# Kernel optimization log

Measured on AMD Instinct MI355X. Metric: run time of the kernel, lower is better.

Reference implementation:

```python
import jax, jax.numpy as jnp
import numpy as np

N_NODES = 100000
N_EDGES = 3200000


def _spmm(edge_row, edge_col, edge_val, h):
    # out[i] = sum_{e: row[e]==i} val[e] * h[col[e]]
    msgs = edge_val[:, None] * h[edge_col]  # [E, F]
    return jax.ops.segment_sum(msgs, edge_row, num_segments=N_NODES)


def _gc_layer(x, W, b, edge_row, edge_col, edge_val):
    # GraphConvolution: support = x @ W; out = spmm(adj, support) + b
    support = x @ W
    return _spmm(edge_row, edge_col, edge_val, support) + b


def setup_inputs() -> dict:
    key = jax.random.key(0)
    ks = jax.random.split(key, 8)
    F_IN, HID, C = 512, 256, 40
    x = jax.random.normal(ks[0], (N_NODES, F_IN), dtype=jnp.float32)
    W1 = jax.random.normal(ks[1], (F_IN, HID), dtype=jnp.float32) * (1.0 / np.sqrt(F_IN))
    b1 = jnp.zeros((HID,), dtype=jnp.float32)
    W2 = jax.random.normal(ks[2], (HID, C), dtype=jnp.float32) * (1.0 / np.sqrt(HID))
    b2 = jnp.zeros((C,), dtype=jnp.float32)
    edge_row = jax.random.randint(ks[3], (N_EDGES,), 0, N_NODES, dtype=jnp.int32)
    edge_col = jax.random.randint(ks[4], (N_EDGES,), 0, N_NODES, dtype=jnp.int32)
    edge_val = jax.random.uniform(ks[5], (N_EDGES,), dtype=jnp.float32) * 0.05
    return {"x": x, "W1": W1, "b1": b1, "W2": W2, "b2": b2,
            "edge_row": edge_row, "edge_col": edge_col, "edge_val": edge_val}


def reference(x, W1, b1, W2, b2, edge_row, edge_col, edge_val):
    h = jax.nn.relu(_gc_layer(x, W1, b1, edge_row, edge_col, edge_val))
    # dropout: inference mode (training=False) -> identity
    logits = _gc_layer(h, W2, b2, edge_row, edge_col, edge_val)
    return (jax.nn.log_softmax(logits, axis=1), jax.nn.softmax(logits, axis=1))
```

## Files before the change

### kernel.cpp

```cpp
#include <hip/hip_runtime.h>
#include <hip/hip_bf16.h>

#define N_NODES 100000
#define N_EDGES 3200000
#define F_IN    512
#define HID     256
#define C_OUT   40

#define RPB     512
#define BSHIFT  9
#define NBUCK   196
#define CAP     20480
#define GSTR    16

typedef unsigned short u16;
typedef unsigned char  u8;
typedef unsigned int   u32;
typedef __attribute__((ext_vector_type(8))) short bf16x8;
typedef __attribute__((ext_vector_type(4))) float f32x4;
typedef __attribute__((ext_vector_type(2))) float f32x2;

__device__ __forceinline__ u16 f2bf(float f) {
    u32 x = __float_as_uint(f);
    return (u16)((x + 0x7fffu + ((x >> 16) & 1u)) >> 16);
}
__device__ __forceinline__ u32 pk2(float lo, float hi) {
    return (u32)f2bf(lo) | ((u32)f2bf(hi) << 16);
}


__global__ __launch_bounds__(256) void k_prep(const float* __restrict__ W1,
                                              const float* __restrict__ W2,
                                              u16* __restrict__ W1t,
                                              u16* __restrict__ W2t,
                                              int* __restrict__ gfill) {
    int b = blockIdx.x, t = threadIdx.x;
    if (b < 512) {
        int i = b * 256 + t;
        int k = i >> 8, n = i & 255;
        W1t[(size_t)n * F_IN + k] = f2bf(W1[i]);
    } else if (b < 576) {
        int i = (b - 512) * 256 + t;
        int n = i >> 8, k = i & 255;
        W2t[i] = (n < C_OUT) ? f2bf(W2[k * C_OUT + n]) : (u16)0;
    } else {
        for (int j = t; j < NBUCK * GSTR; j += 256) gfill[j] = 0;
    }
}


__global__ __launch_bounds__(1024) void k_p1(const int* __restrict__ row,
                                             const int* __restrict__ col,
                                             const float* __restrict__ val,
                                             int* __restrict__ gfill,
                                             int2* __restrict__ bpack) {
    __shared__ int hist[NBUCK];
    __shared__ int base[NBUCK];
    int t = threadIdx.x;
    for (int j = t; j < NBUCK; j += 1024) hist[j] = 0;
    __syncthreads();
    int e0 = blockIdx.x * 4096;
    int bin[4], key[4], lr[4];
    float vl[4];
#pragma unroll
    for (int u = 0; u < 4; u++) {
        int i = e0 + u * 1024 + t;
        if (i < N_EDGES) {
            int r = row[i];
            bin[u] = r >> BSHIFT;
            key[u] = (col[i] << BSHIFT) | (r & (RPB - 1));
            vl[u] = val[i];
            lr[u] = atomicAdd(&hist[bin[u]], 1);
        } else {
            bin[u] = -1;
        }
    }
    __syncthreads();
    for (int j = t; j < NBUCK; j += 1024)
        base[j] = atomicAdd(&gfill[j * GSTR], hist[j]);
    __syncthreads();
#pragma unroll
    for (int u = 0; u < 4; u++) {
        if (bin[u] >= 0) {
            int p = base[bin[u]] + lr[u];
            if (p < CAP)
                bpack[(size_t)bin[u] * CAP + p] = make_int2(key[u], __float_as_int(vl[u]));
        }
    }
}

__global__ __launch_bounds__(1024) void k_p2(const int2* __restrict__ bpack,
                                             const int* __restrict__ gfill,
                                             int2* __restrict__ cpack,
                                             int* __restrict__ row_off) {
    __shared__ int bb[256];
    __shared__ int cnt[RPB];
    __shared__ int sc[RPB];
    __shared__ int rbase[RPB];
    int b = blockIdx.x, t = threadIdx.x;
    if (t < 256) bb[t] = (t < NBUCK) ? gfill[t * GSTR] : 0;
    __syncthreads();
    for (int off = 1; off < 256; off <<= 1) {
        int x = 0;
        if (t < 256 && t >= off) x = bb[t - off];
        __syncthreads();
        if (t < 256) bb[t] += x;
        __syncthreads();
    }
    int gbase = (b == 0) ? 0 : bb[b - 1];
    if (b == NBUCK - 1 && t == 0) row_off[N_NODES] = bb[NBUCK - 1];
    int n = gfill[b * GSTR];
    if (n > CAP) n = CAP;
    if (t < RPB) cnt[t] = 0;
    __syncthreads();
    int key[20], lr[20];
    float v[20];
#pragma unroll
    for (int u = 0; u < 20; u++) {
        int i = u * 1024 + t;
        if (i < n) {
            int2 p = bpack[(size_t)b * CAP + i];
            key[u] = p.x;
            v[u] = __int_as_float(p.y);
            lr[u] = atomicAdd(&cnt[key[u] & (RPB - 1)], 1);
        } else {
            key[u] = -1;
        }
    }
    __syncthreads();
    if (t < RPB) sc[t] = cnt[t];
    __syncthreads();
    for (int off = 1; off < RPB; off <<= 1) {
        int x = 0;
        if (t < RPB && t >= off) x = sc[t - off];
        __syncthreads();
        if (t < RPB) sc[t] += x;
        __syncthreads();
    }
    if (t < RPB) rbase[t] = (t == 0) ? 0 : sc[t - 1];
    __syncthreads();
    int g0 = b * RPB;
    if (t < RPB && (g0 + t) < N_NODES) row_off[g0 + t] = gbase + rbase[t];
#pragma unroll
    for (int u = 0; u < 20; u++) {
        if (key[u] >= 0) {
            int pos = gbase + rbase[key[u] & (RPB - 1)] + lr[u];
            cpack[pos] = make_int2(key[u] >> BSHIFT, __float_as_int(v[u]));
        }
    }
}


#define ASTR 40
#define BSTR 40

__global__ __launch_bounds__(512) void k_gemm1(const float* __restrict__ A,
                                               const u16* __restrict__ Bt,
                                               u8* __restrict__ Cf8, int M) {
    __shared__ u16 As[2][128 * ASTR];
    __shared__ u16 Bs[2][256 * BSTR];
    int tid = threadIdx.x;
    int bm = blockIdx.x * 128;
    int lane = tid & 63, wid = tid >> 6;
    int wm = wid >> 2, wn = wid & 3;

    int s_ar = tid >> 2;
    int s_ak = (tid & 3) * 8;
    int s_bn = tid >> 1;
    int s_bk = (tid & 1) * 16;

    bool arow_ok = (bm + s_ar) < M;
    const float* aptr = A + (size_t)(bm + s_ar) * F_IN + s_ak;
    const u16*   bptr = Bt + (size_t)s_bn * F_IN + s_bk;

    f32x4 acc[4][4];
#pragma unroll
    for (int i = 0; i < 4; i++)
#pragma unroll
        for (int j = 0; j < 4; j++) acc[i][j] = (f32x4){0.f, 0.f, 0.f, 0.f};

    float4 ra0, ra1;
    int4 rb0, rb1;

    auto LOAD = [&](int kt) {
        const float* ap = aptr + kt * 32;
        if (arow_ok) {
            ra0 = *(const float4*)ap;
            ra1 = *(const float4*)(ap + 4);
        } else {
            ra0 = make_float4(0.f, 0.f, 0.f, 0.f);
            ra1 = ra0;
        }
        const u16* bp = bptr + kt * 32;
        rb0 = *(const int4*)bp;
        rb1 = *(const int4*)(bp + 8);
    };
    auto WRITE = [&](int buf) {
        int4 w;
        w.x = pk2(ra0.x, ra0.y);
        w.y = pk2(ra0.z, ra0.w);
        w.z = pk2(ra1.x, ra1.y);
        w.w = pk2(ra1.z, ra1.w);
        *(int4*)&As[buf][s_ar * ASTR + s_ak] = w;
        *(int4*)&Bs[buf][s_bn * BSTR + s_bk] = rb0;
        *(int4*)&Bs[buf][s_bn * BSTR + s_bk + 8] = rb1;
    };

    int kg = lane >> 4;
    int r16 = lane & 15;

    auto COMPUTE = [&](int buf) {
        bf16x8 a[4], b[4];
#pragma unroll
        for (int mt = 0; mt < 4; mt++)
            a[mt] = *(const bf16x8*)&As[buf][(wm * 64 + mt * 16 + r16) * ASTR + kg * 8];
#pragma unroll
        for (int nt = 0; nt < 4; nt++)
            b[nt] = *(const bf16x8*)&Bs[buf][(wn * 64 + nt * 16 + r16) * BSTR + kg * 8];
#pragma unroll
        for (int mt = 0; mt < 4; mt++)
#pragma unroll
            for (int nt = 0; nt < 4; nt++)
                acc[mt][nt] = __builtin_amdgcn_mfma_f32_16x16x32_bf16(
                    b[nt], a[mt], acc[mt][nt], 0, 0, 0);
    };

    LOAD(0);
    WRITE(0);
    __syncthreads();
#pragma unroll 1
    for (int kt = 0; kt < F_IN / 32; kt++) {
        int cur = kt & 1;
        if (kt < F_IN / 32 - 1) LOAD(kt + 1);
        COMPUTE(cur);
        if (kt < F_IN / 32 - 1) WRITE(cur ^ 1);
        __syncthreads();
    }

#pragma unroll
    for (int mt = 0; mt < 4; mt++) {
        int xr = bm + wm * 64 + mt * 16 + (lane & 15);
        if (xr < M) {
#pragma unroll
            for (int nt = 0; nt < 4; nt++) {
                int wc0 = wn * 64 + nt * 16 + (lane >> 4) * 4;
                u32 d = __builtin_amdgcn_cvt_pk_fp8_f32(acc[mt][nt][0], acc[mt][nt][1], 0u, false);
                d = __builtin_amdgcn_cvt_pk_fp8_f32(acc[mt][nt][2], acc[mt][nt][3], d, true);
                *(u32*)&Cf8[(size_t)xr * HID + wc0] = d;
            }
        }
    }
}


__global__ __launch_bounds__(256) void k_spmm1(const u8* __restrict__ Sf8,
                                               const int2* __restrict__ cpack,
                                               const int* __restrict__ row_off,
                                               const float* __restrict__ b1,
                                               u8* __restrict__ Hb8) {
    int lane = threadIdx.x & 63;
    int row = blockIdx.x * 4 + (threadIdx.x >> 6);
    int beg = __builtin_amdgcn_readfirstlane(row_off[row]);
    int end = __builtin_amdgcn_readfirstlane(row_off[row + 1]);
    int f4 = lane * 4;
    const u8* base = Sf8 + f4;
    float acc[4] = {};
    int e = beg;
    for (; e + 8 <= end; e += 8) {
        int2 q[8];
#pragma unroll
        for (int t = 0; t < 8; t++) q[t] = cpack[e + t];
#pragma unroll
        for (int t = 0; t < 8; t++) {
            float vv = __int_as_float(q[t].y);
            u32 w = *(const u32*)(base + (size_t)q[t].x * HID);
            f32x2 lo = __builtin_amdgcn_cvt_pk_f32_fp8(w, false);
            f32x2 hi = __builtin_amdgcn_cvt_pk_f32_fp8(w, true);
            acc[0] += vv * lo.x;
            acc[1] += vv * lo.y;
            acc[2] += vv * hi.x;
            acc[3] += vv * hi.y;
        }
    }
    for (; e < end; e++) {
        int2 q = cpack[e];
        float vv = __int_as_float(q.y);
        u32 w = *(const u32*)(base + (size_t)q.x * HID);
        f32x2 lo = __builtin_amdgcn_cvt_pk_f32_fp8(w, false);
        f32x2 hi = __builtin_amdgcn_cvt_pk_f32_fp8(w, true);
        acc[0] += vv * lo.x;
        acc[1] += vv * lo.y;
        acc[2] += vv * hi.x;
        acc[3] += vv * hi.y;
    }
    float4 b = *(const float4*)&b1[f4];
    float h0 = fmaxf(acc[0] + b.x, 0.f);
    float h1 = fmaxf(acc[1] + b.y, 0.f);
    float h2 = fmaxf(acc[2] + b.z, 0.f);
    float h3 = fmaxf(acc[3] + b.w, 0.f);
    u32 d = __builtin_amdgcn_cvt_pk_fp8_f32(h0, h1, 0u, false);
    d = __builtin_amdgcn_cvt_pk_fp8_f32(h2, h3, d, true);
    *(u32*)&Hb8[(size_t)row * HID + f4] = d;
}


#define G2STR 264

__global__ __launch_bounds__(256) void k_gemm2(const u8* __restrict__ Hb8,
                                               const u16* __restrict__ W2t,
                                               u8* __restrict__ S2f8) {
    __shared__ u16 As[64 * G2STR];
    int tid = threadIdx.x;
    int base = blockIdx.x * 64;
    {
        int r = tid >> 2, c0 = (tid & 3) * 64;
        const u8* src = Hb8 + (size_t)(base + r) * HID + c0;
        bool ok = (base + r) < N_NODES;
#pragma unroll
        for (int q = 0; q < 4; q++) {
            uint4 dv = ok ? *(const uint4*)(src + q * 16) : make_uint4(0, 0, 0, 0);
            u32 wbuf[8];
            u32 dd[4] = {dv.x, dv.y, dv.z, dv.w};
#pragma unroll
            for (int j = 0; j < 4; j++) {
                f32x2 lo = __builtin_amdgcn_cvt_pk_f32_fp8(dd[j], false);
                f32x2 hi = __builtin_amdgcn_cvt_pk_f32_fp8(dd[j], true);
                wbuf[2 * j]     = pk2(lo.x, lo.y);
                wbuf[2 * j + 1] = pk2(hi.x, hi.y);
            }
            *(int4*)&As[r * G2STR + c0 + q * 16]     = *(int4*)&wbuf[0];
            *(int4*)&As[r * G2STR + c0 + q * 16 + 8] = *(int4*)&wbuf[4];
        }
    }
    __syncthreads();
    int lane = tid & 63, wv = tid >> 6;
    int r16 = lane & 15, kg = lane >> 4;
    f32x4 acc[4];
#pragma unroll
    for (int nt = 0; nt < 4; nt++) acc[nt] = (f32x4){0.f, 0.f, 0.f, 0.f};
#pragma unroll
    for (int ks = 0; ks < 8; ks++) {
        bf16x8 a = *(const bf16x8*)&As[(wv * 16 + r16) * G2STR + ks * 32 + kg * 8];
#pragma unroll
        for (int nt = 0; nt < 4; nt++) {
            bf16x8 b = *(const bf16x8*)&W2t[(size_t)(nt * 16 + r16) * 256 + ks * 32 + kg * 8];
            acc[nt] = __builtin_amdgcn_mfma_f32_16x16x32_bf16(b, a, acc[nt], 0, 0, 0);
        }
    }
    int hr = base + wv * 16 + (lane & 15);
    if (hr < N_NODES) {
#pragma unroll
        for (int nt = 0; nt < 3; nt++) {
            int cls0 = nt * 16 + (lane >> 4) * 4;
            if (cls0 < C_OUT) {
                u32 d = __builtin_amdgcn_cvt_pk_fp8_f32(acc[nt][0], acc[nt][1], 0u, false);
                d = __builtin_amdgcn_cvt_pk_fp8_f32(acc[nt][2], acc[nt][3], d, true);
                *(u32*)&S2f8[(size_t)hr * C_OUT + cls0] = d;
            }
        }
    }
}


__global__ __launch_bounds__(256) void k_spmm2(const u8* __restrict__ S2f8,
                                               const int2* __restrict__ cpack,
                                               const int* __restrict__ row_off,
                                               const float* __restrict__ b2,
                                               float* __restrict__ out_ls,
                                               float* __restrict__ out_sm) {
    __shared__ float red[4][64][4];
    int tid = threadIdx.x;
    int lane = tid & 63, wv = tid >> 6;
    int row = blockIdx.x * 4 + wv;
    int beg = __builtin_amdgcn_readfirstlane(row_off[row]);
    int end = __builtin_amdgcn_readfirstlane(row_off[row + 1]);
    int g = lane / 10;
    int cb = (lane % 10) * 4;
    bool act = lane < 60;
    float acc[4] = {};
    for (int e0 = beg; e0 < end; e0 += 6) {
        int ei = e0 + g;
        bool ok = act && (ei < end);
        int2 q = cpack[ok ? ei : beg];
        float vv = ok ? __int_as_float(q.y) : 0.f;
        u32 w = *(const u32*)(S2f8 + (size_t)q.x * C_OUT + cb);
        f32x2 lo = __builtin_amdgcn_cvt_pk_f32_fp8(w, false);
        f32x2 hi = __builtin_amdgcn_cvt_pk_f32_fp8(w, true);
        acc[0] += vv * lo.x;
        acc[1] += vv * lo.y;
        acc[2] += vv * hi.x;
        acc[3] += vv * hi.y;
    }
#pragma unroll
    for (int j = 0; j < 4; j++) red[wv][lane][j] = acc[j];
    __builtin_amdgcn_s_waitcnt(0);
    float v;
    if (lane < C_OUT) {
        int sl = lane >> 2, j = lane & 3;
        float s = 0.f;
#pragma unroll
        for (int gg = 0; gg < 6; gg++) s += red[wv][gg * 10 + sl][j];
        v = s + b2[lane];
    } else {
        v = -1e30f;
    }
    float mx = v;
    for (int s = 32; s; s >>= 1) mx = fmaxf(mx, __shfl_xor(mx, s));
    float e2 = (lane < C_OUT) ? __expf(v - mx) : 0.f;
    float sum = e2;
    for (int s = 32; s; s >>= 1) sum += __shfl_xor(sum, s);
    float ls = v - mx - __logf(sum);
    float sm = e2 / sum;
    if (lane < C_OUT) {
        out_ls[(size_t)row * C_OUT + lane] = ls;
        out_sm[(size_t)row * C_OUT + lane] = sm;
    }
}


extern "C" void kernel_launch(void* const* d_in, const int* in_sizes, int n_in,
                              void* d_out, int out_size, void* d_ws, size_t ws_size,
                              hipStream_t stream) {
    const float* x    = (const float*)d_in[0];
    const float* W1   = (const float*)d_in[1];
    const float* b1   = (const float*)d_in[2];
    const float* W2   = (const float*)d_in[3];
    const float* b2   = (const float*)d_in[4];
    const int*   erow = (const int*)d_in[5];
    const int*   ecol = (const int*)d_in[6];
    const float* eval = (const float*)d_in[7];
    float* out = (float*)d_out;

    char* w = (char*)d_ws;
    auto alloc = [&](size_t bytes) {
        char* p = w;
        w += (bytes + 255) & ~(size_t)255;
        return p;
    };
    u8*    support = (u8*)   alloc((size_t)N_NODES * HID);
    u8*    hbuf8   = (u8*)   alloc((size_t)N_NODES * HID);
    int2*  cpack   = (int2*) alloc((size_t)N_EDGES * sizeof(int2));
    int2*  bpack   = (int2*) alloc((size_t)NBUCK * CAP * sizeof(int2));
    int*   row_off = (int*)  alloc((size_t)(N_NODES + 1) * sizeof(int));
    int*   gfill   = (int*)  alloc((size_t)NBUCK * GSTR * sizeof(int));
    u8*    S2f8    = (u8*)   alloc((size_t)N_NODES * C_OUT);
    u16*   W2t     = (u16*)  alloc((size_t)64 * 256 * sizeof(u16));
    u16*   W1t     = (u16*)  alloc((size_t)F_IN * HID * sizeof(u16));

    k_prep<<<577, 256, 0, stream>>>(W1, W2, W1t, W2t, gfill);

    int NB1 = (N_EDGES + 4095) / 4096;
    k_p1<<<NB1, 1024, 0, stream>>>(erow, ecol, eval, gfill, bpack);
    k_p2<<<NBUCK, 1024, 0, stream>>>(bpack, gfill, cpack, row_off);

    k_gemm1<<<(N_NODES + 127) / 128, 512, 0, stream>>>(x, W1t, support, N_NODES);
    k_spmm1<<<N_NODES / 4, 256, 0, stream>>>(support, cpack, row_off, b1, hbuf8);
    k_gemm2<<<(N_NODES + 63) / 64, 256, 0, stream>>>(hbuf8, W2t, S2f8);
    k_spmm2<<<N_NODES / 4, 256, 0, stream>>>(S2f8, cpack, row_off, b2,
                                             out, out + (size_t)N_NODES * C_OUT);
}
```

Before: 375.9 us.

## Fuse edge bucketing pass with first GEMM into one interleaved kernel

Merges the edge-bucketing pass (k_p1) and the x@W1 GEMM into a single launch, with odd blocks doing edge partitioning and even blocks doing GEMM tiles. The intent is to overlap the atomic- and scatter-bound bucketing with the bandwidth- and MFMA-bound GEMM and to remove one kernel launch and dependency gap. Partition blocks now use 512 threads handling 8 edges each, and they share the GEMM's 60KB static LDS allocation, which may reduce their occupancy.

After: 402.8 us. 7.2% more time.

```diff
diff --git a/kernel.cpp b/kernel.cpp
--- a/kernel.cpp
+++ b/kernel.cpp
@@ -49,45 +49,152 @@
 }
 
 
-__global__ __launch_bounds__(1024) void k_p1(const int* __restrict__ row,
-                                             const int* __restrict__ col,
-                                             const float* __restrict__ val,
-                                             int* __restrict__ gfill,
-                                             int2* __restrict__ bpack) {
-    __shared__ int hist[NBUCK];
-    __shared__ int base[NBUCK];
-    int t = threadIdx.x;
-    for (int j = t; j < NBUCK; j += 1024) hist[j] = 0;
-    __syncthreads();
-    int e0 = blockIdx.x * 4096;
-    int bin[4], key[4], lr[4];
-    float vl[4];
-#pragma unroll
-    for (int u = 0; u < 4; u++) {
-        int i = e0 + u * 1024 + t;
-        if (i < N_EDGES) {
-            int r = row[i];
-            bin[u] = r >> BSHIFT;
-            key[u] = (col[i] << BSHIFT) | (r & (RPB - 1));
-            vl[u] = val[i];
-            lr[u] = atomicAdd(&hist[bin[u]], 1);
+#define ASTR 40
+#define BSTR 40
+
+__global__ __launch_bounds__(512) void k_fused1(
+        const int* __restrict__ row, const int* __restrict__ col,
+        const float* __restrict__ val,
+        int* __restrict__ gfill, int2* __restrict__ bpack,
+        const float* __restrict__ A, const u16* __restrict__ Bt,
+        u8* __restrict__ Cf8, int M) {
+    __shared__ __align__(16) char smem[61440];
+    int tid = threadIdx.x;
+
+    if (blockIdx.x & 1) {
+        int* hist = (int*)smem;
+        int* base = hist + NBUCK;
+        int pb = blockIdx.x >> 1;
+        for (int j = tid; j < NBUCK; j += 512) hist[j] = 0;
+        __syncthreads();
+        int e0 = pb * 4096;
+        int bin[8], key[8], lr[8];
+        float vl[8];
+#pragma unroll
+        for (int u = 0; u < 8; u++) {
+            int i = e0 + u * 512 + tid;
+            if (i < N_EDGES) {
+                int r = row[i];
+                bin[u] = r >> BSHIFT;
+                key[u] = (col[i] << BSHIFT) | (r & (RPB - 1));
+                vl[u] = val[i];
+                lr[u] = atomicAdd(&hist[bin[u]], 1);
+            } else {
+                bin[u] = -1;
+            }
+        }
+        __syncthreads();
+        for (int j = tid; j < NBUCK; j += 512)
+            base[j] = atomicAdd(&gfill[j * GSTR], hist[j]);
+        __syncthreads();
+#pragma unroll
+        for (int u = 0; u < 8; u++) {
+            if (bin[u] >= 0) {
+                int p = base[bin[u]] + lr[u];
+                if (p < CAP)
+                    bpack[(size_t)bin[u] * CAP + p] =
+                        make_int2(key[u], __float_as_int(vl[u]));
+            }
+        }
+        return;
+    }
+
+    u16* As = (u16*)smem;
+    u16* Bs = (u16*)(smem + 20480);
+    int bm = (blockIdx.x >> 1) * 128;
+    int lane = tid & 63, wid = tid >> 6;
+    int wm = wid >> 2, wn = wid & 3;
+
+    int s_ar = tid >> 2;
+    int s_ak = (tid & 3) * 8;
+    int s_bn = tid >> 1;
+    int s_bk = (tid & 1) * 16;
+
+    bool arow_ok = (bm + s_ar) < M;
+    const float* aptr = A + (size_t)(bm + s_ar) * F_IN + s_ak;
+    const u16*   bptr = Bt + (size_t)s_bn * F_IN + s_bk;
+
+    f32x4 acc[4][4];
+#pragma unroll
+    for (int i = 0; i < 4; i++)
+#pragma unroll
+        for (int j = 0; j < 4; j++) acc[i][j] = (f32x4){0.f, 0.f, 0.f, 0.f};
+
+    float4 ra0, ra1;
+    int4 rb0, rb1;
+
+    auto LOAD = [&](int kt) {
+        const float* ap = aptr + kt * 32;
+        if (arow_ok) {
+            ra0 = *(const float4*)ap;
+            ra1 = *(const float4*)(ap + 4);
         } else {
-            bin[u] = -1;
-        }
-    }
-    __syncthreads();
-    for (int j = t; j < NBUCK; j += 1024)
-        base[j] = atomicAdd(&gfill[j * GSTR], hist[j]);
-    __syncthreads();
-#pragma unroll
-    for (int u = 0; u < 4; u++) {
-        if (bin[u] >= 0) {
-            int p = base[bin[u]] + lr[u];
-            if (p < CAP)
-                bpack[(size_t)bin[u] * CAP + p] = make_int2(key[u], __float_as_int(vl[u]));
-        }
-    }
-}
+            ra0 = make_float4(0.f, 0.f, 0.f, 0.f);
+            ra1 = ra0;
+        }
+        const u16* bp = bptr + kt * 32;
+        rb0 = *(const int4*)bp;
+        rb1 = *(const int4*)(bp + 8);
+    };
+    auto WRITE = [&](int buf) {
+        int4 w;
+        w.x = pk2(ra0.x, ra0.y);
+        w.y = pk2(ra0.z, ra0.w);
+        w.z = pk2(ra1.x, ra1.y);
+        w.w = pk2(ra1.z, ra1.w);
+        *(int4*)&As[buf * (128 * ASTR) + s_ar * ASTR + s_ak] = w;
+        *(int4*)&Bs[buf * (256 * BSTR) + s_bn * BSTR + s_bk] = rb0;
+        *(int4*)&Bs[buf * (256 * BSTR) + s_bn * BSTR + s_bk + 8] = rb1;
+    };
+
+    int kg = lane >> 4;
+    int r16 = lane & 15;
+
+    auto COMPUTE = [&](int buf) {
+        bf16x8 a[4], b[4];
+#pragma unroll
+        for (int mt = 0; mt < 4; mt++)
+            a[mt] = *(const bf16x8*)&As[buf * (128 * ASTR) +
+                                        (wm * 64 + mt * 16 + r16) * ASTR + kg * 8];
+#pragma unroll
+        for (int nt = 0; nt < 4; nt++)
+            b[nt] = *(const bf16x8*)&Bs[buf * (256 * BSTR) +
+                                        (wn * 64 + nt * 16 + r16) * BSTR + kg * 8];
+#pragma unroll
+        for (int mt = 0; mt < 4; mt++)
+#pragma unroll
+            for (int nt = 0; nt < 4; nt++)
+                acc[mt][nt] = __builtin_amdgcn_mfma_f32_16x16x32_bf16(
+                    b[nt], a[mt], acc[mt][nt], 0, 0, 0);
+    };
+
+    LOAD(0);
+    WRITE(0);
+    __syncthreads();
+#pragma unroll 1
+    for (int kt = 0; kt < F_IN / 32; kt++) {
+        int cur = kt & 1;
+        if (kt < F_IN / 32 - 1) LOAD(kt + 1);
+        COMPUTE(cur);
+        if (kt < F_IN / 32 - 1) WRITE(cur ^ 1);
+        __syncthreads();
+    }
+
+#pragma unroll
+    for (int mt = 0; mt < 4; mt++) {
+        int xr = bm + wm * 64 + mt * 16 + (lane & 15);
+        if (xr < M) {
+#pragma unroll
+            for (int nt = 0; nt < 4; nt++) {
+                int wc0 = wn * 64 + nt * 16 + (lane >> 4) * 4;
+                u32 d = __builtin_amdgcn_cvt_pk_fp8_f32(acc[mt][nt][0], acc[mt][nt][1], 0u, false);
+                d = __builtin_amdgcn_cvt_pk_fp8_f32(acc[mt][nt][2], acc[mt][nt][3], d, true);
+                *(u32*)&Cf8[(size_t)xr * HID + wc0] = d;
+            }
+        }
+    }
+}
+
 
 __global__ __launch_bounds__(1024) void k_p2(const int2* __restrict__ bpack,
                                              const int* __restrict__ gfill,
@@ -146,108 +253,6 @@
         if (key[u] >= 0) {
             int pos = gbase + rbase[key[u] & (RPB - 1)] + lr[u];
             cpack[pos] = make_int2(key[u] >> BSHIFT, __float_as_int(v[u]));
-        }
-    }
-}
-
-
-#define ASTR 40
-#define BSTR 40
-
-__global__ __launch_bounds__(512) void k_gemm1(const float* __restrict__ A,
-                                               const u16* __restrict__ Bt,
-                                               u8* __restrict__ Cf8, int M) {
-    __shared__ u16 As[2][128 * ASTR];
-    __shared__ u16 Bs[2][256 * BSTR];
-    int tid = threadIdx.x;
-    int bm = blockIdx.x * 128;
-    int lane = tid & 63, wid = tid >> 6;
-    int wm = wid >> 2, wn = wid & 3;
-
-    int s_ar = tid >> 2;
-    int s_ak = (tid & 3) * 8;
-    int s_bn = tid >> 1;
-    int s_bk = (tid & 1) * 16;
-
-    bool arow_ok = (bm + s_ar) < M;
-    const float* aptr = A + (size_t)(bm + s_ar) * F_IN + s_ak;
-    const u16*   bptr = Bt + (size_t)s_bn * F_IN + s_bk;
-
-    f32x4 acc[4][4];
-#pragma unroll
-    for (int i = 0; i < 4; i++)
-#pragma unroll
-        for (int j = 0; j < 4; j++) acc[i][j] = (f32x4){0.f, 0.f, 0.f, 0.f};
-
-    float4 ra0, ra1;
-    int4 rb0, rb1;
-
-    auto LOAD = [&](int kt) {
-        const float* ap = aptr + kt * 32;
-        if (arow_ok) {
-            ra0 = *(const float4*)ap;
-            ra1 = *(const float4*)(ap + 4);
-        } else {
-            ra0 = make_float4(0.f, 0.f, 0.f, 0.f);
-            ra1 = ra0;
-        }
-        const u16* bp = bptr + kt * 32;
-        rb0 = *(const int4*)bp;
-        rb1 = *(const int4*)(bp + 8);
-    };
-    auto WRITE = [&](int buf) {
-        int4 w;
-        w.x = pk2(ra0.x, ra0.y);
-        w.y = pk2(ra0.z, ra0.w);
-        w.z = pk2(ra1.x, ra1.y);
-        w.w = pk2(ra1.z, ra1.w);
-        *(int4*)&As[buf][s_ar * ASTR + s_ak] = w;
-        *(int4*)&Bs[buf][s_bn * BSTR + s_bk] = rb0;
-        *(int4*)&Bs[buf][s_bn * BSTR + s_bk + 8] = rb1;
-    };
-
-    int kg = lane >> 4;
-    int r16 = lane & 15;
-
-    auto COMPUTE = [&](int buf) {
-        bf16x8 a[4], b[4];
-#pragma unroll
-        for (int mt = 0; mt < 4; mt++)
-            a[mt] = *(const bf16x8*)&As[buf][(wm * 64 + mt * 16 + r16) * ASTR + kg * 8];
-#pragma unroll
-        for (int nt = 0; nt < 4; nt++)
-            b[nt] = *(const bf16x8*)&Bs[buf][(wn * 64 + nt * 16 + r16) * BSTR + kg * 8];
-#pragma unroll
-        for (int mt = 0; mt < 4; mt++)
-#pragma unroll
-            for (int nt = 0; nt < 4; nt++)
-                acc[mt][nt] = __builtin_amdgcn_mfma_f32_16x16x32_bf16(
-                    b[nt], a[mt], acc[mt][nt], 0, 0, 0);
-    };
-
-    LOAD(0);
-    WRITE(0);
-    __syncthreads();
-#pragma unroll 1
-    for (int kt = 0; kt < F_IN / 32; kt++) {
-        int cur = kt & 1;
-        if (kt < F_IN / 32 - 1) LOAD(kt + 1);
-        COMPUTE(cur);
-        if (kt < F_IN / 32 - 1) WRITE(cur ^ 1);
-        __syncthreads();
-    }
-
-#pragma unroll
-    for (int mt = 0; mt < 4; mt++) {
-        int xr = bm + wm * 64 + mt * 16 + (lane & 15);
-        if (xr < M) {
-#pragma unroll
-            for (int nt = 0; nt < 4; nt++) {
-                int wc0 = wn * 64 + nt * 16 + (lane >> 4) * 4;
-                u32 d = __builtin_amdgcn_cvt_pk_fp8_f32(acc[mt][nt][0], acc[mt][nt][1], 0u, false);
-                d = __builtin_amdgcn_cvt_pk_fp8_f32(acc[mt][nt][2], acc[mt][nt][3], d, true);
-                *(u32*)&Cf8[(size_t)xr * HID + wc0] = d;
-            }
         }
     }
 }
@@ -449,11 +454,10 @@
 
     k_prep<<<577, 256, 0, stream>>>(W1, W2, W1t, W2t, gfill);
 
-    int NB1 = (N_EDGES + 4095) / 4096;
-    k_p1<<<NB1, 1024, 0, stream>>>(erow, ecol, eval, gfill, bpack);
+    k_fused1<<<1564, 512, 0, stream>>>(erow, ecol, eval, gfill, bpack,
+                                       x, W1t, support, N_NODES);
     k_p2<<<NBUCK, 1024, 0, stream>>>(bpack, gfill, cpack, row_off);
 
-    k_gemm1<<<(N_NODES + 127) / 128, 512, 0, stream>>>(x, W1t, support, N_NODES);
     k_spmm1<<<N_NODES / 4, 256, 0, stream>>>(support, cpack, row_off, b1, hbuf8);
     k_gemm2<<<(N_NODES + 63) / 64, 256, 0, stream>>>(hbuf8, W2t, S2f8);
     k_spmm2<<<N_NODES / 4, 256, 0, stream>>>(S2f8, cpack, row_off, b2,
```
